# Kernel tuning notes

Hardware: AMD Instinct MI355X
Metric: run time of the kernel (lower is better)

Reference implementation:

```python
import jax, jax.numpy as jnp
import numpy as np

N, E, C = 20000, 320000, 10000
IN, H, D = 768, 8, 64
HD = H * D
SA_H = 128


def _gat(feat, src, dst, W, al, ar, b):
    # DGL GATConv: fc -> per-node attn terms -> edge leaky_relu -> edge softmax over dst -> scatter-add -> bias -> elu
    h = (feat @ W).reshape(N, H, D)                       # [N,H,D]
    el = (h * al).sum(-1)                                 # [N,H]
    er = (h * ar).sum(-1)                                 # [N,H]
    e = jax.nn.leaky_relu(el[src] + er[dst], 0.2)         # [E,H]
    m = jax.ops.segment_max(e, dst, num_segments=N)       # [N,H]
    m = jnp.where(jnp.isfinite(m), m, 0.0)                # zero in-degree nodes
    ee = jnp.exp(e - m[dst])                              # [E,H]
    denom = jax.ops.segment_sum(ee, dst, num_segments=N)  # [N,H]
    a = ee / jnp.maximum(denom[dst], 1e-9)                # [E,H]
    out = jax.ops.segment_sum(a[:, :, None] * h[src], dst, num_segments=N)  # [N,H,D]
    return jax.nn.elu(out + b.reshape(1, H, D))


def _sem(z, w1, b1, w2):
    # SemanticAttention: per-metapath score -> softmax over metapaths -> weighted sum
    w = (jnp.tanh(z @ w1 + b1) @ w2).mean(0)              # [M,1]
    beta = jax.nn.softmax(w, axis=0)                      # [M,1]
    return (beta[None] * z).sum(1)                        # [C,HD]


def setup_inputs():
    key = jax.random.key(0)
    ks = jax.random.split(key, 32)
    inp = {}
    for i in range(3):
        inp[f"feat{i}"] = jax.random.normal(ks[i], (N, IN), jnp.float32)
        inp[f"src{i}"] = jax.random.randint(ks[3 + i], (E,), 0, N, dtype=jnp.int32)
        inp[f"dst{i}"] = jax.random.randint(ks[6 + i], (E,), 0, N, dtype=jnp.int32)
        inp[f"char{i}"] = jnp.arange(C, dtype=jnp.int32)
        inp[f"W{i}"] = jax.random.normal(ks[9 + i], (IN, HD), jnp.float32) * 0.05
        inp[f"al{i}"] = jax.random.normal(ks[12 + i], (H, D), jnp.float32) * 0.05
        inp[f"ar{i}"] = jax.random.normal(ks[15 + i], (H, D), jnp.float32) * 0.05
        inp[f"b{i}"] = jnp.zeros((HD,), jnp.float32)
    inp["sw1"] = jax.random.normal(ks[18], (HD, SA_H), jnp.float32) * 0.05
    inp["sb1"] = jnp.zeros((SA_H,), jnp.float32)
    inp["sw2"] = jax.random.normal(ks[19], (SA_H, 1), jnp.float32) * 0.05
    inp["aw1"] = jax.random.normal(ks[20], (HD, SA_H), jnp.float32) * 0.05
    inp["ab1"] = jnp.zeros((SA_H,), jnp.float32)
    inp["aw2"] = jax.random.normal(ks[21], (SA_H, 1), jnp.float32) * 0.05
    return inp


def reference(feat0, feat1, feat2, src0, src1, src2, dst0, dst1, dst2, char0, char1, char2,
              W0, W1, W2, al0, al1, al2, ar0, ar1, ar2, b0, b1, b2,
              sw1, sb1, sw2, aw1, ab1, aw2):
    h1 = _gat(feat0, src0, dst0, W0, al0, ar0, b0)        # [N,H,D]
    hh = _gat(feat2, src2, dst2, W2, al2, ar2, b2)        # [N,H,D]
    z = jnp.stack([h1[char0].reshape(C, HD), hh[char2].reshape(C, HD)], axis=1)  # [C,2,HD]
    sound = _sem(z, sw1, sb1, sw2)                        # [C,HD]
    h2 = _gat(feat1, src1, dst1, W1, al1, ar1, b1)        # [N,H,D]
    z2 = jnp.stack([sound, h2[char1].reshape(C, HD)], axis=1)  # [C,2,HD]
    sem_emb = _sem(z2, aw1, ab1, aw2).reshape(C, H, D)    # [C,H,D]
    h1 = h1.at[char0].set(sem_emb)
    h2 = h2.at[char1].set(sem_emb)
    hh = hh.at[char2].set(sem_emb)
    return sem_emb, h1.mean(1), h2.mean(1), hh.mean(1)
```

## Files before the change

kernel.cpp:

```cpp
#include <hip/hip_runtime.h>
#include <math.h>

#define NN 20000
#define NE 320000
#define CC 10000
#define KIN 768
#define NH 8
#define ND 64
#define NHD 512
#define NSA 128
#define NBKT 79

#define WTB_SZ (NHD * KIN)
#define W1TB_SZ (NSA * NHD)
#define APAD 136
#define GB 1280

typedef __attribute__((ext_vector_type(4))) float f32x4;
typedef __attribute__((ext_vector_type(8))) short s16x8;

__device__ __forceinline__ unsigned short f2bf(float f) {
  unsigned u = __float_as_uint(f);
  u += 0x7fffu + ((u >> 16) & 1u);
  return (unsigned short)(u >> 16);
}
__device__ __forceinline__ float bf2f(unsigned short s) {
  return __uint_as_float(((unsigned)s) << 16);
}
__device__ __forceinline__ float bflo(unsigned u) { return __uint_as_float(u << 16); }
__device__ __forceinline__ float bfhi(unsigned u) { return __uint_as_float(u & 0xffff0000u); }

__device__ __forceinline__ void gl_lds16(const void* g, void* l) {
  __builtin_amdgcn_global_load_lds(
      (const __attribute__((address_space(1))) unsigned int*)g,
      (__attribute__((address_space(3))) unsigned int*)l, 16, 0, 0);
}

__global__ void k_prep(const float* __restrict__ W0, const float* __restrict__ W1,
                       const float* __restrict__ W2, const float* __restrict__ sw1,
                       const float* __restrict__ aw1, unsigned short* __restrict__ wtb3,
                       unsigned short* __restrict__ w1tb2, int* __restrict__ deg3,
                       float* __restrict__ scal) {
  int i = blockIdx.x * 256 + threadIdx.x;
  if (i < 3 * WTB_SZ) {
    int g = i / WTB_SZ;
    int j = i - g * WTB_SZ;
    int n = j / KIN, k = j - n * KIN;
    const float* W = (g == 0) ? W0 : (g == 1) ? W1 : W2;
    wtb3[i] = f2bf(W[(size_t)k * NHD + n]);
    return;
  }
  i -= 3 * WTB_SZ;
  if (i < 2 * W1TB_SZ) {
    int p = i / W1TB_SZ;
    int j = i - p * W1TB_SZ;
    int n = j / NHD, k = j - n * NHD;
    const float* W = p ? aw1 : sw1;
    w1tb2[p * W1TB_SZ + n * NHD + k] = f2bf(W[(size_t)k * NSA + n]);
    return;
  }
  i -= 2 * W1TB_SZ;
  if (i < 3 * NN) { deg3[i] = 0; return; }
  i -= 3 * NN;
  if (i < 4) scal[i] = 0.f;
}

__global__ __launch_bounds__(256, 2) void k_gemm_gat3(
    const float* __restrict__ f0, const float* __restrict__ f1, const float* __restrict__ f2,
    const unsigned short* __restrict__ wtb3, unsigned short* __restrict__ hb3,
    const float* __restrict__ al0, const float* __restrict__ al1, const float* __restrict__ al2,
    const float* __restrict__ ar0, const float* __restrict__ ar1, const float* __restrict__ ar2,
    float* __restrict__ el3, float* __restrict__ er3) {
  __shared__ unsigned short As[64 * APAD];
  __shared__ unsigned short Bs[128 * 128];
  const int bidg = blockIdx.x;
  const int g = bidg / GB;
  const int bid = bidg - g * GB;
  const int xcd = bidg & 7, t = bid >> 3;
  const int rowblk = (t >> 2) * 8 + xcd;
  if (rowblk * 64 >= NN) return;
  const float* A = (g == 0) ? f0 : (g == 1) ? f1 : f2;
  const float* al = (g == 0) ? al0 : (g == 1) ? al1 : al2;
  const float* ar = (g == 0) ? ar0 : (g == 1) ? ar1 : ar2;
  const unsigned short* Bt = wtb3 + (size_t)g * WTB_SZ;
  unsigned short* outb = hb3 + (size_t)g * NN * NHD;
  float* el = el3 + (size_t)g * NN * NH;
  float* er = er3 + (size_t)g * NN * NH;

  const int row0 = rowblk * 64;
  const int col0 = (t & 3) * 128;
  const int tid = threadIdx.x;
  const int wv = tid >> 6, lane = tid & 63;
  const int wr = (wv & 1) * 32, wc = (wv >> 1) * 64;

  f32x4 acc[2][4] = {};

  const int l15 = lane & 15;
  const int q = lane >> 4;

  const int arow = tid >> 2, ci = tid & 3;
  int aga = row0 + arow; if (aga > NN - 1) aga = NN - 1;
  const float* ap = A + (size_t)aga * KIN;

  const int binrow = lane >> 4, bch = lane & 15;

  for (int k0 = 0; k0 < KIN; k0 += 128) {
#pragma unroll
    for (int j = 0; j < 8; j++) {
      int rb0 = (wv * 8 + j) * 4;
      int grow = col0 + rb0 + binrow;
      int srcch = bch ^ ((j & 3) * 4 + binrow);
      gl_lds16(Bt + (size_t)grow * KIN + k0 + srcch * 8, Bs + rb0 * 128);
    }
#pragma unroll
    for (int sc = 0; sc < 4; sc++) {
      int s = ci + sc * 4;
      const float* sp = ap + k0 + s * 8;
      float4 fa = ((const float4*)sp)[0];
      float4 fb = ((const float4*)sp)[1];
      uint4 pk;
      pk.x = ((unsigned)f2bf(fa.y) << 16) | f2bf(fa.x);
      pk.y = ((unsigned)f2bf(fa.w) << 16) | f2bf(fa.z);
      pk.z = ((unsigned)f2bf(fb.y) << 16) | f2bf(fb.x);
      pk.w = ((unsigned)f2bf(fb.w) << 16) | f2bf(fb.z);
      *(uint4*)(As + arow * APAD + s * 8) = pk;
    }
    __syncthreads();
#pragma unroll
    for (int kk = 0; kk < 4; kk++) {
      s16x8 af[2], bf4[4];
#pragma unroll
      for (int m = 0; m < 2; m++) {
        int r = wr + m * 16 + l15;
        af[m] = *(const s16x8*)(As + r * APAD + (kk * 4 + q) * 8);
      }
#pragma unroll
      for (int n = 0; n < 4; n++) {
        int rB = wc + n * 16 + l15;
        int slot = (kk * 4 + q) ^ l15;
        bf4[n] = *(const s16x8*)(Bs + rB * 128 + slot * 8);
      }
#pragma unroll
      for (int m = 0; m < 2; m++)
#pragma unroll
        for (int n = 0; n < 4; n++)
          acc[m][n] = __builtin_amdgcn_mfma_f32_16x16x32_bf16(af[m], bf4[n], acc[m][n], 0, 0, 0);
    }
    __syncthreads();
  }

  const int cbase = col0 + wc + l15;
  const int rq = (lane >> 4) * 4;
  const int hd = (col0 + wc) >> 6;
  float alc[4], arc[4];
#pragma unroll
  for (int n = 0; n < 4; n++) { alc[n] = al[cbase + n * 16]; arc[n] = ar[cbase + n * 16]; }

#pragma unroll
  for (int m = 0; m < 2; m++) {
#pragma unroll
    for (int r = 0; r < 4; r++) {
      int grow = row0 + wr + m * 16 + rq + r;
      float a = 0.f, b = 0.f;
#pragma unroll
      for (int n = 0; n < 4; n++) {
        float v = acc[m][n][r];
        a += v * alc[n];
        b += v * arc[n];
      }
      a += __shfl_xor(a, 1, 64); a += __shfl_xor(a, 2, 64);
      a += __shfl_xor(a, 4, 64); a += __shfl_xor(a, 8, 64);
      b += __shfl_xor(b, 1, 64); b += __shfl_xor(b, 2, 64);
      b += __shfl_xor(b, 4, 64); b += __shfl_xor(b, 8, 64);
      if (grow < NN) {
        unsigned short* dp = outb + (size_t)grow * NHD + cbase;
#pragma unroll
        for (int n = 0; n < 4; n++) dp[n * 16] = f2bf(acc[m][n][r]);
        if (l15 == 0) {
          el[(size_t)grow * NH + hd] = a;
          er[(size_t)grow * NH + hd] = b;
        }
      }
    }
  }
}

__global__ __launch_bounds__(256, 2) void k_gemm_sem(const unsigned short* __restrict__ A0,
                                                     const unsigned short* __restrict__ A1,
                                                     const unsigned short* __restrict__ Bt,
                                                     const float* __restrict__ b1,
                                                     const float* __restrict__ w2,
                                                     float* __restrict__ scal) {
  __shared__ unsigned short As[128 * 32];
  __shared__ unsigned short Bs[128 * 32];
  __shared__ float rsum[2][128];
  __shared__ float pp[2][2];
  const int M = 2 * CC;
  const int tid = threadIdx.x;
  const int wv = tid >> 6, lane = tid & 63;
  const int row0 = blockIdx.x * 128;
  const int wr = (wv >> 1) * 64, wc = (wv & 1) * 64;
  const int ci = lane & 3, rsub = lane >> 2;

  f32x4 acc[4][4] = {};

  const int l15 = lane & 15;
  const int pc = (((lane >> 4) ^ ((l15 >> 1) & 3))) * 8;

  for (int k0 = 0; k0 < NHD; k0 += 32) {
#pragma unroll
    for (int i = 0; i < 2; i++) {
      int lrow = (wv * 2 + i) * 16 + rsub;
      int kc = (ci ^ ((lrow >> 1) & 3)) << 3;
      int ga = row0 + lrow; if (ga > M - 1) ga = M - 1;
      const unsigned short* Ap = (ga < CC) ? A0 + (size_t)ga * NHD
                                           : A1 + (size_t)(ga - CC) * NHD;
      gl_lds16(Ap + k0 + kc, As + (wv * 2 + i) * 512);
      int gb = lrow;
      gl_lds16(Bt + (size_t)gb * NHD + k0 + kc, Bs + (wv * 2 + i) * 512);
    }
    __syncthreads();
    s16x8 af[4], bf[4];
#pragma unroll
    for (int m = 0; m < 4; m++) {
      af[m] = *(const s16x8*)(As + (wr + m * 16 + l15) * 32 + pc);
      bf[m] = *(const s16x8*)(Bs + (wc + m * 16 + l15) * 32 + pc);
    }
#pragma unroll
    for (int m = 0; m < 4; m++)
#pragma unroll
      for (int n = 0; n < 4; n++)
        acc[m][n] = __builtin_amdgcn_mfma_f32_16x16x32_bf16(af[m], bf[n], acc[m][n], 0, 0, 0);
    __syncthreads();
  }

  if (tid < 128) { rsum[0][tid] = 0.f; rsum[1][tid] = 0.f; }
  __syncthreads();
  const int cb = wc + l15;
  const int rq = (lane >> 4) * 4;
  float b1c[4], w2c[4];
#pragma unroll
  for (int n = 0; n < 4; n++) { b1c[n] = b1[cb + n * 16]; w2c[n] = w2[cb + n * 16]; }
#pragma unroll
  for (int m = 0; m < 4; m++) {
#pragma unroll
    for (int r = 0; r < 4; r++) {
      int rl = wr + m * 16 + rq + r;
      float s = 0.f;
#pragma unroll
      for (int n = 0; n < 4; n++) s += tanhf(acc[m][n][r] + b1c[n]) * w2c[n];
      s += __shfl_xor(s, 1, 64); s += __shfl_xor(s, 2, 64);
      s += __shfl_xor(s, 4, 64); s += __shfl_xor(s, 8, 64);
      if (l15 == 0 && row0 + rl < M) rsum[wv & 1][rl] = s;
    }
  }
  __syncthreads();
  if (tid < 128) {
    int grow = row0 + tid;
    float v = rsum[0][tid] + rsum[1][tid];
    float vA = (grow < CC) ? v : 0.f;
    float vB = (grow >= CC && grow < M) ? v : 0.f;
#pragma unroll
    for (int off = 32; off > 0; off >>= 1) {
      vA += __shfl_xor(vA, off, 64);
      vB += __shfl_xor(vB, off, 64);
    }
    if ((tid & 63) == 0) { pp[tid >> 6][0] = vA; pp[tid >> 6][1] = vB; }
  }
  __syncthreads();
  if (tid == 0) {
    atomicAdd(scal + 0, pp[0][0] + pp[1][0]);
    atomicAdd(scal + 1, pp[0][1] + pp[1][1]);
  }
}

__global__ void k_hist3(const int* __restrict__ d0, const int* __restrict__ d1,
                        const int* __restrict__ d2, int* __restrict__ deg3) {
  int e = blockIdx.x * 256 + threadIdx.x;
  int g = blockIdx.y;
  const int* dst = (g == 0) ? d0 : (g == 1) ? d1 : d2;
  atomicAdd(deg3 + g * NN + dst[e], 1);
}

__global__ __launch_bounds__(1024) void k_scan3(const int* __restrict__ deg3,
                                                int* __restrict__ rowptr3,
                                                int* __restrict__ curB) {
  __shared__ int part[1024];
  const int g = blockIdx.x;
  const int* deg = deg3 + g * NN;
  int* rowptr = rowptr3 + g * (NN + 1);
  int tid = threadIdx.x;
  const int CH = 20;
  int base = tid * CH;
  int s = 0;
  for (int i = 0; i < CH; i++) { int idx = base + i; if (idx < NN) s += deg[idx]; }
  part[tid] = s;
  __syncthreads();
  for (int off = 1; off < 1024; off <<= 1) {
    int u = (tid >= off) ? part[tid - off] : 0;
    int v = part[tid];
    __syncthreads();
    part[tid] = u + v;
    __syncthreads();
  }
  int run = (tid == 0) ? 0 : part[tid - 1];
  for (int i = 0; i < CH; i++) {
    int idx = base + i;
    if (idx < NN) {
      rowptr[idx] = run;
      if ((idx & 255) == 0) curB[g * (NBKT + 1) + (idx >> 8)] = run;
      run += deg[idx];
    }
  }
  if (tid == 1023) rowptr[NN] = part[1023];
}

__global__ __launch_bounds__(1024) void k_coarse(const int* __restrict__ s0,
                                                 const int* __restrict__ s1,
                                                 const int* __restrict__ s2,
                                                 const int* __restrict__ d0,
                                                 const int* __restrict__ d1,
                                                 const int* __restrict__ d2,
                                                 int* __restrict__ curB,
                                                 unsigned* __restrict__ staging) {
  __shared__ int bcnt[NBKT];
  __shared__ int bbase[NBKT];
  int g = blockIdx.y;
  const int* src = (g == 0) ? s0 : (g == 1) ? s1 : s2;
  const int* dst = (g == 0) ? d0 : (g == 1) ? d1 : d2;
  int tid = threadIdx.x;
  if (tid < NBKT) bcnt[tid] = 0;
  __syncthreads();
  int e = blockIdx.x * 1024 + tid;
  bool val = e < NE;
  int b = 0, r = 0, sv = 0, dv = 0;
  if (val) {
    dv = dst[e]; sv = src[e];
    b = dv >> 8;
    r = atomicAdd(&bcnt[b], 1);
  }
  __syncthreads();
  if (tid < NBKT && bcnt[tid] > 0) bbase[tid] = atomicAdd(&curB[g * (NBKT + 1) + tid], bcnt[tid]);
  __syncthreads();
  if (val) staging[(size_t)g * NE + bbase[b] + r] = ((unsigned)sv << 8) | (unsigned)(dv & 255);
}

__global__ __launch_bounds__(1024) void k_fine(const int* __restrict__ rowptr3,
                                               const unsigned* __restrict__ staging,
                                               unsigned short* __restrict__ srcord3) {
  __shared__ int cur[256];
  int g = blockIdx.y, b = blockIdx.x;
  const int* rowptr = rowptr3 + g * (NN + 1);
  int n0 = b << 8;
  int tid = threadIdx.x;
  if (tid < 256) {
    int node = n0 + tid;
    cur[tid] = (node < NN) ? rowptr[node] : 0;
  }
  __syncthreads();
  int nend = n0 + 256; if (nend > NN) nend = NN;
  int start = rowptr[n0];
  int endp = rowptr[nend];
  for (int i = start + tid; i < endp; i += 1024) {
    unsigned u = staging[(size_t)g * NE + i];
    int nl = u & 255;
    int pos = atomicAdd(&cur[nl], 1);
    srcord3[(size_t)g * NE + pos] = (unsigned short)(u >> 8);
  }
}

__global__ __launch_bounds__(256) void k_aggf3(const int* __restrict__ rowptr3,
                                               const unsigned short* __restrict__ srcord3,
                                               const float* __restrict__ el3,
                                               const float* __restrict__ er3,
                                               const unsigned short* __restrict__ hb3,
                                               const float* __restrict__ b0p,
                                               const float* __restrict__ b1p,
                                               const float* __restrict__ b2p,
                                               unsigned short* __restrict__ ob3) {
  __shared__ float aS[4][64 * 8];
  __shared__ int sS[4][64];
  int g = blockIdx.y;
  const int* rowptr = rowptr3 + g * (NN + 1);
  const unsigned short* srcord = srcord3 + (size_t)g * NE;
  const float* el = el3 + (size_t)g * NN * NH;
  const float* er = er3 + (size_t)g * NN * NH;
  const unsigned short* hb = hb3 + (size_t)g * NN * NHD;
  const float* bias = (g == 0) ? b0p : (g == 1) ? b1p : b2p;
  unsigned short* ob = ob3 + (size_t)g * NN * NHD;

  int wv = threadIdx.x >> 6;
  int t = (blockIdx.x * 256 + threadIdx.x) >> 6;
  int lane = threadIdx.x & 63;
  int h = lane >> 3;
  int beg = rowptr[t], end = rowptr[t + 1];

  float4 er0 = ((const float4*)(er + (size_t)t * NH))[0];
  float4 er1 = ((const float4*)(er + (size_t)t * NH))[1];
  float erow[8] = {er0.x, er0.y, er0.z, er0.w, er1.x, er1.y, er1.z, er1.w};

  float acc[8] = {0.f, 0.f, 0.f, 0.f, 0.f, 0.f, 0.f, 0.f};
  float den = 0.f;

  for (int cbeg = beg; cbeg < end; cbeg += 64) {
    int cnt = end - cbeg; if (cnt > 64) cnt = 64;
    bool valid = lane < cnt;
    int pidx = cbeg + lane; if (pidx > end - 1) pidx = end - 1;
    int s = srcord[pidx];
    if (valid) {
      sS[wv][lane] = s;
      float4 a0 = ((const float4*)(el + (size_t)s * NH))[0];
      float4 a1 = ((const float4*)(el + (size_t)s * NH))[1];
      float v[8] = {a0.x + erow[0], a0.y + erow[1], a0.z + erow[2], a0.w + erow[3],
                    a1.x + erow[4], a1.y + erow[5], a1.z + erow[6], a1.w + erow[7]};
#pragma unroll
      for (int k = 0; k < 8; k++) {
        float x = v[k];
        x = x >= 0.f ? x : 0.2f * x;
        aS[wv][lane * 8 + k] = __expf(x);
      }
    }
    const unsigned short* hbl = hb + lane * 8;
    int q = 0;
    for (; q + 3 < cnt; q += 4) {
      int s0 = sS[wv][q], s1 = sS[wv][q + 1], s2 = sS[wv][q + 2], s3 = sS[wv][q + 3];
      float w0 = aS[wv][q * 8 + h];
      float w1 = aS[wv][(q + 1) * 8 + h];
      float w2 = aS[wv][(q + 2) * 8 + h];
      float w3 = aS[wv][(q + 3) * 8 + h];
      uint4 v0 = *(const uint4*)(hbl + (size_t)s0 * NHD);
      uint4 v1 = *(const uint4*)(hbl + (size_t)s1 * NHD);
      uint4 v2 = *(const uint4*)(hbl + (size_t)s2 * NHD);
      uint4 v3 = *(const uint4*)(hbl + (size_t)s3 * NHD);
      den += (w0 + w1) + (w2 + w3);
      acc[0] += w0 * bflo(v0.x); acc[1] += w0 * bfhi(v0.x);
      acc[2] += w0 * bflo(v0.y); acc[3] += w0 * bfhi(v0.y);
      acc[4] += w0 * bflo(v0.z); acc[5] += w0 * bfhi(v0.z);
      acc[6] += w0 * bflo(v0.w); acc[7] += w0 * bfhi(v0.w);
      acc[0] += w1 * bflo(v1.x); acc[1] += w1 * bfhi(v1.x);
      acc[2] += w1 * bflo(v1.y); acc[3] += w1 * bfhi(v1.y);
      acc[4] += w1 * bflo(v1.z); acc[5] += w1 * bfhi(v1.z);
      acc[6] += w1 * bflo(v1.w); acc[7] += w1 * bfhi(v1.w);
      acc[0] += w2 * bflo(v2.x); acc[1] += w2 * bfhi(v2.x);
      acc[2] += w2 * bflo(v2.y); acc[3] += w2 * bfhi(v2.y);
      acc[4] += w2 * bflo(v2.z); acc[5] += w2 * bfhi(v2.z);
      acc[6] += w2 * bflo(v2.w); acc[7] += w2 * bfhi(v2.w);
      acc[0] += w3 * bflo(v3.x); acc[1] += w3 * bfhi(v3.x);
      acc[2] += w3 * bflo(v3.y); acc[3] += w3 * bfhi(v3.y);
      acc[4] += w3 * bflo(v3.z); acc[5] += w3 * bfhi(v3.z);
      acc[6] += w3 * bflo(v3.w); acc[7] += w3 * bfhi(v3.w);
    }
    for (; q < cnt; q++) {
      int s0 = sS[wv][q];
      float w0 = aS[wv][q * 8 + h];
      uint4 v0 = *(const uint4*)(hbl + (size_t)s0 * NHD);
      den += w0;
      acc[0] += w0 * bflo(v0.x); acc[1] += w0 * bfhi(v0.x);
      acc[2] += w0 * bflo(v0.y); acc[3] += w0 * bfhi(v0.y);
      acc[4] += w0 * bflo(v0.z); acc[5] += w0 * bfhi(v0.z);
      acc[6] += w0 * bflo(v0.w); acc[7] += w0 * bfhi(v0.w);
    }
  }

  float dn = 1.f / fmaxf(den, 1e-9f);
  float4 b0 = ((const float4*)(bias + lane * 8))[0];
  float4 b1 = ((const float4*)(bias + lane * 8))[1];
  float r[8];
  r[0] = acc[0] * dn + b0.x; r[1] = acc[1] * dn + b0.y;
  r[2] = acc[2] * dn + b0.z; r[3] = acc[3] * dn + b0.w;
  r[4] = acc[4] * dn + b1.x; r[5] = acc[5] * dn + b1.y;
  r[6] = acc[6] * dn + b1.z; r[7] = acc[7] * dn + b1.w;
#pragma unroll
  for (int j = 0; j < 8; j++) r[j] = r[j] > 0.f ? r[j] : expm1f(r[j]);
  uint4 z;
  z.x = ((unsigned)f2bf(r[1]) << 16) | f2bf(r[0]);
  z.y = ((unsigned)f2bf(r[3]) << 16) | f2bf(r[2]);
  z.z = ((unsigned)f2bf(r[5]) << 16) | f2bf(r[4]);
  z.w = ((unsigned)f2bf(r[7]) << 16) | f2bf(r[6]);
  *(uint4*)(ob + (size_t)t * NHD + lane * 8) = z;
}

__global__ void k_combine_s1(const float* __restrict__ scal,
                             const unsigned short* __restrict__ zA,
                             const unsigned short* __restrict__ zB,
                             unsigned short* __restrict__ outb) {
  int i = blockIdx.x * 256 + threadIdx.x;
  float w0 = scal[0] * (1.f / CC), w1v = scal[1] * (1.f / CC);
  float mx = fmaxf(w0, w1v);
  float e0 = expf(w0 - mx), e1 = expf(w1v - mx);
  float inv = 1.f / (e0 + e1);
  float b0 = e0 * inv, b1v = e1 * inv;
  ushort4 a = ((const ushort4*)zA)[i];
  ushort4 b = ((const ushort4*)zB)[i];
  ushort4 z;
  z.x = f2bf(b0 * bf2f(a.x) + b1v * bf2f(b.x));
  z.y = f2bf(b0 * bf2f(a.y) + b1v * bf2f(b.y));
  z.z = f2bf(b0 * bf2f(a.z) + b1v * bf2f(b.z));
  z.w = f2bf(b0 * bf2f(a.w) + b1v * bf2f(b.w));
  ((ushort4*)outb)[i] = z;
}

__global__ void k_comb2_means(const float* __restrict__ scal,
                              const unsigned short* __restrict__ zsound,
                              const unsigned short* __restrict__ ob0,
                              const unsigned short* __restrict__ ob1,
                              const unsigned short* __restrict__ ob2,
                              float* __restrict__ outf,
                              float* __restrict__ m1, float* __restrict__ m2,
                              float* __restrict__ m3) {
  int idx = blockIdx.x * 256 + threadIdx.x;
  int n = idx >> 6, d = idx & 63;
  if (n < CC) {
    float w0 = scal[0] * (1.f / CC), w1v = scal[1] * (1.f / CC);
    float mx = fmaxf(w0, w1v);
    float e0 = expf(w0 - mx), e1 = expf(w1v - mx);
    float inv = 1.f / (e0 + e1);
    float b0 = e0 * inv, b1v = e1 * inv;
    const unsigned short* zs = zsound + (size_t)n * NHD + d;
    const unsigned short* p1 = ob1 + (size_t)n * NHD + d;
    float* po = outf + (size_t)n * NHD + d;
    float v = 0.f;
#pragma unroll
    for (int h = 0; h < 8; h++) {
      float r = b0 * bf2f(zs[h * 64]) + b1v * bf2f(p1[h * 64]);
      po[h * 64] = r;
      v += r;
    }
    v *= 0.125f;
    m1[idx] = v; m2[idx] = v; m3[idx] = v;
  } else {
    const unsigned short* p0 = ob0 + (size_t)n * NHD + d;
    const unsigned short* p1 = ob1 + (size_t)n * NHD + d;
    const unsigned short* p2 = ob2 + (size_t)n * NHD + d;
    float v0 = 0.f, v1 = 0.f, v2 = 0.f;
#pragma unroll
    for (int h = 0; h < 8; h++) {
      v0 += bf2f(p0[h * 64]); v1 += bf2f(p1[h * 64]); v2 += bf2f(p2[h * 64]);
    }
    m1[idx] = v0 * 0.125f; m2[idx] = v1 * 0.125f; m3[idx] = v2 * 0.125f;
  }
}

extern "C" void kernel_launch(void* const* d_in, const int* in_sizes, int n_in,
                              void* d_out, int out_size, void* d_ws, size_t ws_size,
                              hipStream_t stream) {
  (void)in_sizes; (void)n_in; (void)out_size; (void)ws_size;

  const float* feat[3]; const int* srcp[3]; const int* dstp[3];
  const float* Wp[3]; const float* alp[3]; const float* arp[3]; const float* bp[3];
  for (int g = 0; g < 3; g++) {
    const int base = g * 8;
    feat[g] = (const float*)d_in[base + 0];
    srcp[g] = (const int*)d_in[base + 1];
    dstp[g] = (const int*)d_in[base + 2];
    Wp[g]   = (const float*)d_in[base + 4];
    alp[g]  = (const float*)d_in[base + 5];
    arp[g]  = (const float*)d_in[base + 6];
    bp[g]   = (const float*)d_in[base + 7];
  }
  const float* sw1 = (const float*)d_in[24];
  const float* sb1 = (const float*)d_in[25];
  const float* sw2 = (const float*)d_in[26];
  const float* aw1 = (const float*)d_in[27];
  const float* ab1 = (const float*)d_in[28];
  const float* aw2 = (const float*)d_in[29];

  char* wsp = (char*)d_ws;
  auto alloc = [&](size_t bytes) {
    char* p = wsp;
    wsp += (bytes + 255) & ~(size_t)255;
    return p;
  };
  unsigned short* ob3 = (unsigned short*)alloc((size_t)3 * NN * NHD * 2);
  unsigned short* hb3 = (unsigned short*)alloc((size_t)3 * NN * NHD * 2);
  unsigned short* wtb3 = (unsigned short*)alloc((size_t)3 * WTB_SZ * 2);
  unsigned short* w1tb2 = (unsigned short*)alloc((size_t)2 * W1TB_SZ * 2);
  unsigned short* sound = (unsigned short*)alloc((size_t)CC * NHD * 2);
  float* el3 = (float*)alloc((size_t)3 * NN * NH * 4);
  float* er3 = (float*)alloc((size_t)3 * NN * NH * 4);
  float* scal = (float*)alloc(256);
  int* deg3 = (int*)alloc((size_t)3 * NN * 4);
  int* rowptr3 = (int*)alloc((size_t)3 * (NN + 1) * 4 + 64);
  int* curB = (int*)alloc((size_t)3 * (NBKT + 1) * 4);
  unsigned* staging = (unsigned*)alloc((size_t)3 * NE * 4);
  unsigned short* srcord3 = (unsigned short*)alloc((size_t)3 * NE * 2);

  unsigned short* ob0 = ob3;
  unsigned short* ob1 = ob3 + (size_t)NN * NHD;
  unsigned short* ob2 = ob3 + (size_t)2 * NN * NHD;

  float* outf = (float*)d_out;
  float* outm1 = outf + (size_t)CC * NHD;
  float* outm2 = outm1 + (size_t)NN * ND;
  float* outm3 = outm2 + (size_t)NN * ND;

  const int PREP_T = 3 * WTB_SZ + 2 * W1TB_SZ + 3 * NN + 4;
  k_prep<<<(PREP_T + 255) / 256, 256, 0, stream>>>(Wp[0], Wp[1], Wp[2], sw1, aw1,
                                                   wtb3, w1tb2, deg3, scal);
  k_hist3<<<dim3(NE / 256, 3), 256, 0, stream>>>(dstp[0], dstp[1], dstp[2], deg3);
  k_scan3<<<3, 1024, 0, stream>>>(deg3, rowptr3, curB);
  k_coarse<<<dim3((NE + 1023) / 1024, 3), 1024, 0, stream>>>(
      srcp[0], srcp[1], srcp[2], dstp[0], dstp[1], dstp[2], curB, staging);
  k_fine<<<dim3(NBKT, 3), 1024, 0, stream>>>(rowptr3, staging, srcord3);

  k_gemm_gat3<<<3 * GB, 256, 0, stream>>>(feat[0], feat[1], feat[2], wtb3, hb3,
                                          alp[0], alp[1], alp[2], arp[0], arp[1], arp[2],
                                          el3, er3);
  k_aggf3<<<dim3(NN * 64 / 256, 3), 256, 0, stream>>>(rowptr3, srcord3, el3, er3, hb3,
                                                      bp[0], bp[1], bp[2], ob3);

  k_gemm_sem<<<(2 * CC + 127) / 128, 256, 0, stream>>>(ob0, ob2, w1tb2, sb1, sw2, scal);
  k_combine_s1<<<CC * NHD / 4 / 256, 256, 0, stream>>>(scal, ob0, ob2, sound);

  k_gemm_sem<<<(2 * CC + 127) / 128, 256, 0, stream>>>(sound, ob1, w1tb2 + W1TB_SZ, ab1, aw2, scal + 2);
  k_comb2_means<<<NN * 64 / 256, 256, 0, stream>>>(scal + 2, sound, ob0, ob1, ob2,
                                                   outf, outm1, outm2, outm3);
}
```

Measured before the change: 411.0 us.

## Retile semantic-attention GEMM to 64-row blocks with 128-deep K steps

The semantic-attention GEMM now uses 64-row output tiles instead of 128, which doubles the block count to 313 so more CUs have work. K is staged 128 at a time with an XOR-swizzled LDS layout, cutting the number of barrier rounds from 16 to 4 per block. The final reduction is simplified to one warp issuing the atomics. LDS use per block grows to about 48KB, which may limit occupancy, and each block reloads the whole B matrix, raising L2 traffic.

```diff
diff --git a/kernel.cpp b/kernel.cpp
--- a/kernel.cpp
+++ b/kernel.cpp
@@ -185,56 +185,70 @@
   }
 }
 
-__global__ __launch_bounds__(256, 2) void k_gemm_sem(const unsigned short* __restrict__ A0,
-                                                     const unsigned short* __restrict__ A1,
-                                                     const unsigned short* __restrict__ Bt,
-                                                     const float* __restrict__ b1,
-                                                     const float* __restrict__ w2,
-                                                     float* __restrict__ scal) {
-  __shared__ unsigned short As[128 * 32];
-  __shared__ unsigned short Bs[128 * 32];
-  __shared__ float rsum[2][128];
-  __shared__ float pp[2][2];
+__global__ __launch_bounds__(256, 2) void k_gemm_sem64(const unsigned short* __restrict__ A0,
+                                                       const unsigned short* __restrict__ A1,
+                                                       const unsigned short* __restrict__ Bt,
+                                                       const float* __restrict__ b1,
+                                                       const float* __restrict__ w2,
+                                                       float* __restrict__ scal) {
+  __shared__ unsigned short As[64 * 128];
+  __shared__ unsigned short Bs[128 * 128];
+  __shared__ float rsum[2][64];
   const int M = 2 * CC;
+  const int row0 = blockIdx.x * 64;
   const int tid = threadIdx.x;
   const int wv = tid >> 6, lane = tid & 63;
-  const int row0 = blockIdx.x * 128;
-  const int wr = (wv >> 1) * 64, wc = (wv & 1) * 64;
-  const int ci = lane & 3, rsub = lane >> 2;
-
-  f32x4 acc[4][4] = {};
+  const int wr = (wv & 1) * 32, wc = (wv >> 1) * 64;
+
+  f32x4 acc[2][4] = {};
 
   const int l15 = lane & 15;
-  const int pc = (((lane >> 4) ^ ((l15 >> 1) & 3))) * 8;
-
-  for (int k0 = 0; k0 < NHD; k0 += 32) {
-#pragma unroll
-    for (int i = 0; i < 2; i++) {
-      int lrow = (wv * 2 + i) * 16 + rsub;
-      int kc = (ci ^ ((lrow >> 1) & 3)) << 3;
-      int ga = row0 + lrow; if (ga > M - 1) ga = M - 1;
+  const int q = lane >> 4;
+  const int binrow = lane >> 4, bch = lane & 15;
+
+  for (int k0 = 0; k0 < NHD; k0 += 128) {
+#pragma unroll
+    for (int j = 0; j < 4; j++) {
+      int rb0 = (wv * 4 + j) * 4;
+      int ga = row0 + rb0 + binrow; if (ga > M - 1) ga = M - 1;
       const unsigned short* Ap = (ga < CC) ? A0 + (size_t)ga * NHD
                                            : A1 + (size_t)(ga - CC) * NHD;
-      gl_lds16(Ap + k0 + kc, As + (wv * 2 + i) * 512);
-      int gb = lrow;
-      gl_lds16(Bt + (size_t)gb * NHD + k0 + kc, Bs + (wv * 2 + i) * 512);
+      int srcch = bch ^ ((j & 3) * 4 + binrow);
+      gl_lds16(Ap + k0 + srcch * 8, As + rb0 * 128);
+    }
+#pragma unroll
+    for (int j = 0; j < 8; j++) {
+      int rb0 = (wv * 8 + j) * 4;
+      int grow = rb0 + binrow;
+      int srcch = bch ^ ((j & 3) * 4 + binrow);
+      gl_lds16(Bt + (size_t)grow * NHD + k0 + srcch * 8, Bs + rb0 * 128);
     }
     __syncthreads();
-    s16x8 af[4], bf[4];
-#pragma unroll
-    for (int m = 0; m < 4; m++) {
-      af[m] = *(const s16x8*)(As + (wr + m * 16 + l15) * 32 + pc);
-      bf[m] = *(const s16x8*)(Bs + (wc + m * 16 + l15) * 32 + pc);
-    }
-#pragma unroll
-    for (int m = 0; m < 4; m++)
-#pragma unroll
-      for (int n = 0; n < 4; n++)
-        acc[m][n] = __builtin_amdgcn_mfma_f32_16x16x32_bf16(af[m], bf[n], acc[m][n], 0, 0, 0);
+#pragma unroll
+    for (int kk = 0; kk < 4; kk++) {
+      s16x8 af[2], bf4[4];
+#pragma unroll
+      for (int m = 0; m < 2; m++) {
+        int r = wr + m * 16 + l15;
+        int slot = (kk * 4 + q) ^ l15;
+        af[m] = *(const s16x8*)(As + r * 128 + slot * 8);
+      }
+#pragma unroll
+      for (int n = 0; n < 4; n++) {
+        int rB = wc + n * 16 + l15;
+        int slot = (kk * 4 + q) ^ l15;
+        bf4[n] = *(const s16x8*)(Bs + rB * 128 + slot * 8);
+      }
+#pragma unroll
+      for (int m = 0; m < 2; m++)
+#pragma unroll
+        for (int n = 0; n < 4; n++)
+          acc[m][n] = __builtin_amdgcn_mfma_f32_16x16x32_bf16(af[m], bf4[n], acc[m][n], 0, 0, 0);
+    }
     __syncthreads();
   }
 
-  if (tid < 128) { rsum[0][tid] = 0.f; rsum[1][tid] = 0.f; }
+  if (tid < 64) { rsum[0][tid] = 0.f; rsum[1][tid] = 0.f; }
   __syncthreads();
   const int cb = wc + l15;
   const int rq = (lane >> 4) * 4;
@@ -242,7 +256,7 @@
 #pragma unroll
   for (int n = 0; n < 4; n++) { b1c[n] = b1[cb + n * 16]; w2c[n] = w2[cb + n * 16]; }
 #pragma unroll
-  for (int m = 0; m < 4; m++) {
+  for (int m = 0; m < 2; m++) {
 #pragma unroll
     for (int r = 0; r < 4; r++) {
       int rl = wr + m * 16 + rq + r;
@@ -251,11 +265,11 @@
       for (int n = 0; n < 4; n++) s += tanhf(acc[m][n][r] + b1c[n]) * w2c[n];
       s += __shfl_xor(s, 1, 64); s += __shfl_xor(s, 2, 64);
       s += __shfl_xor(s, 4, 64); s += __shfl_xor(s, 8, 64);
-      if (l15 == 0 && row0 + rl < M) rsum[wv & 1][rl] = s;
+      if (l15 == 0) rsum[wv >> 1][rl] = s;
     }
   }
   __syncthreads();
-  if (tid < 128) {
+  if (tid < 64) {
     int grow = row0 + tid;
     float v = rsum[0][tid] + rsum[1][tid];
     float vA = (grow < CC) ? v : 0.f;
@@ -265,12 +279,10 @@
       vA += __shfl_xor(vA, off, 64);
       vB += __shfl_xor(vB, off, 64);
     }
-    if ((tid & 63) == 0) { pp[tid >> 6][0] = vA; pp[tid >> 6][1] = vB; }
-  }
-  __syncthreads();
-  if (tid == 0) {
-    atomicAdd(scal + 0, pp[0][0] + pp[1][0]);
-    atomicAdd(scal + 1, pp[0][1] + pp[1][1]);
+    if (tid == 0) {
+      atomicAdd(scal + 0, vA);
+      atomicAdd(scal + 1, vB);
+    }
   }
 }
 
@@ -609,10 +621,10 @@
   k_aggf3<<<dim3(NN * 64 / 256, 3), 256, 0, stream>>>(rowptr3, srcord3, el3, er3, hb3,
                                                       bp[0], bp[1], bp[2], ob3);
 
-  k_gemm_sem<<<(2 * CC + 127) / 128, 256, 0, stream>>>(ob0, ob2, w1tb2, sb1, sw2, scal);
+  k_gemm_sem64<<<(2 * CC + 63) / 64, 256, 0, stream>>>(ob0, ob2, w1tb2, sb1, sw2, scal);
   k_combine_s1<<<CC * NHD / 4 / 256, 256, 0, stream>>>(scal, ob0, ob2, sound);
 
-  k_gemm_sem<<<(2 * CC + 127) / 128, 256, 0, stream>>>(sound, ob1, w1tb2 + W1TB_SZ, ab1, aw2, scal + 2);
+  k_gemm_sem64<<<(2 * CC + 63) / 64, 256, 0, stream>>>(sound, ob1, w1tb2 + W1TB_SZ, ab1, aw2, scal + 2);
   k_comb2_means<<<NN * 64 / 256, 256, 0, stream>>>(scal + 2, sound, ob0, ob1, ob2,
                                                    outf, outm1, outm2, outm3);
 }
```

After: 399.7 us. 2.7% less time.
